# Optimization experiments

Hardware: AMD Instinct MI355X
Metric: run time of the kernel (lower is better)

Reference implementation:

```python
import jax, jax.numpy as jnp
import numpy as np


def _gcn_conv(x, W, b, src, dst, num_nodes):
    # PyG GCNConv: h = x @ W; symmetric normalization with self-loops; scatter-add; + bias
    h = x @ W
    deg = jax.ops.segment_sum(jnp.ones_like(dst, dtype=h.dtype), dst, num_segments=num_nodes)
    dinv = jnp.where(deg > 0, jax.lax.rsqrt(deg), 0.0)
    norm = dinv[src] * dinv[dst]                         # [E]
    msgs = h[src] * norm[:, None]                        # [E, H] gather + scale
    out = jax.ops.segment_sum(msgs, dst, num_segments=num_nodes)
    return out + b


def setup_inputs() -> dict:
    key = jax.random.key(0)
    ks = jax.random.split(key, 10)
    N, E = 500000, 1000000
    IN, H, SIG = 3, 64, 24
    x = jax.random.uniform(ks[0], (N, IN), dtype=jnp.float32)
    edge_index = jax.random.randint(ks[1], (2, E), 0, N, dtype=jnp.int64)
    batch = jnp.zeros((N,), dtype=jnp.int64)
    def glorot(k, shape):
        lim = np.sqrt(6.0 / (shape[0] + shape[1]))
        return jax.random.uniform(k, shape, dtype=jnp.float32, minval=-lim, maxval=lim)
    return {
        "x": x,
        "edge_index": edge_index,
        "batch": batch,
        "W1": glorot(ks[2], (IN, H)), "b1": jnp.zeros((H,), jnp.float32),
        "W2": glorot(ks[3], (H, H)),  "b2": jnp.zeros((H,), jnp.float32),
        "W3": glorot(ks[4], (H, H)),  "b3": jnp.zeros((H,), jnp.float32),
        "Wfc": glorot(ks[5], (H, SIG)), "bfc": jnp.zeros((SIG,), jnp.float32),
    }


def reference(x, edge_index, batch, W1, b1, W2, b2, W3, b3, Wfc, bfc):
    N = x.shape[0]
    NUM_GRAPHS = 1  # batch is all zeros (single graph)
    # add self-loops once (GCNConv adds them per layer; identical edge set each layer)
    loop = jnp.arange(N, dtype=edge_index.dtype)
    src = jnp.concatenate([edge_index[0], loop])
    dst = jnp.concatenate([edge_index[1], loop])

    h = jax.nn.relu(_gcn_conv(x, W1, b1, src, dst, N))
    h = jax.nn.relu(_gcn_conv(h, W2, b2, src, dst, N))
    h = jax.nn.relu(_gcn_conv(h, W3, b3, src, dst, N))

    # global mean pool per graph
    sums = jax.ops.segment_sum(h, batch, num_segments=NUM_GRAPHS)          # [G, H]
    counts = jax.ops.segment_sum(jnp.ones((N,), h.dtype), batch, num_segments=NUM_GRAPHS)
    sig = sums / jnp.maximum(counts, 1.0)[:, None]

    return jnp.tanh(sig @ Wfc + bfc)  # [G, 24]
```

## Files before the change

### kernel.cpp

```cpp
#include <hip/hip_runtime.h>
#include <hip/hip_bf16.h>
#include <hip/hip_fp16.h>


#define ALIGN256(x) (((x) + 255) & ~(size_t)255)
#define NBUCK_MAX 512

typedef _Float16 half8 __attribute__((ext_vector_type(8)));
typedef _Float16 half4 __attribute__((ext_vector_type(4)));
typedef float f32x4 __attribute__((ext_vector_type(4)));
typedef int i32x4 __attribute__((ext_vector_type(4)));

__device__ __forceinline__ void dec16(i32x4 r, half8& a, half8& b) {
    i32x4 u, v;
    u.x = (int)(((unsigned)r.x << 8) & 0xFF00FF00u);
    u.y = (int)(((unsigned)r.x)      & 0xFF00FF00u);
    u.z = (int)(((unsigned)r.y << 8) & 0xFF00FF00u);
    u.w = (int)(((unsigned)r.y)      & 0xFF00FF00u);
    v.x = (int)(((unsigned)r.z << 8) & 0xFF00FF00u);
    v.y = (int)(((unsigned)r.z)      & 0xFF00FF00u);
    v.z = (int)(((unsigned)r.w << 8) & 0xFF00FF00u);
    v.w = (int)(((unsigned)r.w)      & 0xFF00FF00u);
    a = *(half8*)&u; b = *(half8*)&v;
}

__device__ __forceinline__ unsigned char enc8(float x) {
    unsigned short hb = __half_as_ushort(__float2half(x));
    return (unsigned char)((hb + 0x80u) >> 8);
}

__global__ __launch_bounds__(256) void hist_kernel(const int* __restrict__ ei, int E, int CE, int SH,
                                                   int* __restrict__ cnt_mat,
                                                   float* __restrict__ pool,
                                                   unsigned char* __restrict__ h8a,
                                                   unsigned char* __restrict__ h8b, int N) {
    __shared__ int h[NBUCK_MAX];
    const int t = threadIdx.x, blk = blockIdx.x;
    if (blk == 0) {
        if (t < 64) pool[t] = 0.f;
        if (t < 16) {
            ((int*)(h8a + (size_t)N * 64))[t] = 0;
            ((int*)(h8b + (size_t)N * 64))[t] = 0;
        }
    }
    for (int i = t; i < NBUCK_MAX; i += 256) h[i] = 0;
    __syncthreads();
    const int e0 = blk * CE, e1 = min(E, e0 + CE);
    for (int e = e0 + t; e < e1; e += 256)
        atomicAdd(&h[ei[E + e] >> SH], 1);
    __syncthreads();
    for (int i = t; i < NBUCK_MAX; i += 256) cnt_mat[blk * NBUCK_MAX + i] = h[i];
}

__global__ __launch_bounds__(256) void scan_kernel(const int* __restrict__ cnt_mat,
                                                   int* __restrict__ base_mat,
                                                   int* __restrict__ startb, int nchunk, int NBK) {
    __shared__ int tots[NBUCK_MAX];
    const int t = threadIdx.x;
    for (int j = t; j < NBK; j += 256) {
        int run = 0;
        for (int b = 0; b < nchunk; ++b) {
            int v = cnt_mat[b * NBUCK_MAX + j];
            base_mat[b * NBUCK_MAX + j] = run;
            run += v;
        }
        tots[j] = run;
    }
    __syncthreads();
    if (t == 0) {
        int run = 0;
        for (int j = 0; j < NBK; ++j) { int v = tots[j]; startb[j] = run; run += v; }
        startb[NBK] = run;
    }
}

__global__ __launch_bounds__(256) void scatter_kernel(const int* __restrict__ ei, int E, int CE, int SH,
                                                      const int* __restrict__ base_mat,
                                                      const int* __restrict__ start,
                                                      unsigned* __restrict__ bkt) {
    __shared__ int sbuf[4096];
    __shared__ unsigned short sb[4096];
    __shared__ int lh[NBUCK_MAX];
    __shared__ int lbase[NBUCK_MAX];
    __shared__ int cur[NBUCK_MAX];
    __shared__ int ls[256];
    const int t = threadIdx.x, blk = blockIdx.x;
    for (int i = t; i < NBUCK_MAX; i += 256) { lh[i] = 0; cur[i] = 0; }
    __syncthreads();
    const int e0 = blk * CE, e1 = min(E, e0 + CE);
    for (int e = e0 + t; e < e1; e += 256)
        atomicAdd(&lh[ei[E + e] >> SH], 1);
    __syncthreads();
    int a0 = lh[2 * t], a1 = lh[2 * t + 1];
    ls[t] = a0 + a1;
    __syncthreads();
    if (t == 0) {
        int run = 0;
        for (int k = 0; k < 256; ++k) { int v = ls[k]; ls[k] = run; run += v; }
    }
    __syncthreads();
    lbase[2 * t]     = ls[t];
    lbase[2 * t + 1] = ls[t] + a0;
    __syncthreads();
    const unsigned lowm = (1u << SH) - 1u;
    for (int e = e0 + t; e < e1; e += 256) {
        int s = ei[e], d = ei[E + e];
        int b = d >> SH;
        int r = atomicAdd(&cur[b], 1);
        int slot = lbase[b] + r;
        sbuf[slot] = (int)((((unsigned)d & lowm) << 21) | (unsigned)s);
        sb[slot] = (unsigned short)b;
    }
    __syncthreads();
    const int n = e1 - e0;
    for (int i = t; i < n; i += 256) {
        int b = sb[i];
        int dest = start[b] + base_mat[blk * NBUCK_MAX + b] + (i - lbase[b]);
        bkt[dest] = (unsigned)sbuf[i];
    }
}

__global__ __launch_bounds__(256) void build_kernel(const unsigned* __restrict__ bkt,
                                                    const int* __restrict__ start,
                                                    int SH, int nrows, int N,
                                                    const float* __restrict__ x,
                                                    int* __restrict__ ell, int* __restrict__ sec,
                                                    half4* __restrict__ xs) {
    __shared__ __align__(16) int loc[2048][8];
    const int t = threadIdx.x, j = blockIdx.x;
    const int R = 1 << SH;
    int4 z = make_int4(0, 0, 0, 0);
    for (int i = t; i < R * 2; i += 256) ((int4*)loc)[i] = z;
    __syncthreads();
    const int s0 = start[j], s1 = start[j + 1];
    for (int e = s0 + t; e < s1; e += 256) {
        unsigned p = bkt[e];
        int dl = (int)(p >> 21);
        int src = (int)(p & 0x1FFFFFu);
        int k = atomicAdd(&loc[dl][0], 1);
        if (k < 7) loc[dl][1 + k] = src;
        else if (k < 15) {
            int grow = (j << SH) + dl;
            sec[(size_t)grow * 8 + (k - 7)] = src;
        }
    }
    __syncthreads();
    const int base = j << SH;
    for (int i = t; i < R; i += 256) {
        int grow = base + i;
        if (grow < nrows) {
            int4* dst = (int4*)(ell + (size_t)grow * 8);
            dst[0] = ((int4*)&loc[i][0])[0];
            dst[1] = ((int4*)&loc[i][0])[1];
            if (grow < N) {
                float d = rsqrtf((float)(loc[i][0] + 1));
                half4 v;
                v[0] = (_Float16)(d * x[(size_t)grow * 3 + 0]);
                v[1] = (_Float16)(d * x[(size_t)grow * 3 + 1]);
                v[2] = (_Float16)(d * x[(size_t)grow * 3 + 2]);
                v[3] = (_Float16)0.f;
                xs[grow] = v;
            } else if (grow == N) {
                *(int2*)&xs[N] = make_int2(0, 0);
            }
        }
    }
}

__global__ __launch_bounds__(256) void layer1_kernel(const half4* __restrict__ xs,
                                                     const int* __restrict__ ell,
                                                     const int* __restrict__ sec,
                                                     const float* __restrict__ W1, const float* __restrict__ b1,
                                                     unsigned char* __restrict__ hout, int N) {
    __shared__ float4 a1S[256];
    const int t = threadIdx.x;
    const int jg = blockIdx.x * 256 + t;
    const bool valid = (jg < N);
    const int jc = valid ? jg : N;

    half4 sv = xs[jc];
    float sx = (float)sv[0], sy = (float)sv[1], sz = (float)sv[2];
    const int* row = ell + (size_t)(valid ? jg : 0) * 8;
    int4 e0 = *(const int4*)row;
    int4 e1 = *(const int4*)(row + 4);
    int craw = valid ? e0.x : 0;
    int deg = min(craw, 15);
    int i0 = (deg > 0) ? e0.y : N;
    int i1 = (deg > 1) ? e0.z : N;
    int i2 = (deg > 2) ? e0.w : N;
    int i3 = (deg > 3) ? e1.x : N;
    int i4 = (deg > 4) ? e1.y : N;
    int i5 = (deg > 5) ? e1.z : N;
    int i6 = (deg > 6) ? e1.w : N;
    half4 q0 = xs[i0], q1 = xs[i1], q2 = xs[i2], q3 = xs[i3];
    half4 q4 = xs[i4], q5 = xs[i5], q6 = xs[i6];
    sx += (float)q0[0] + (float)q1[0] + (float)q2[0] + (float)q3[0]
        + (float)q4[0] + (float)q5[0] + (float)q6[0];
    sy += (float)q0[1] + (float)q1[1] + (float)q2[1] + (float)q3[1]
        + (float)q4[1] + (float)q5[1] + (float)q6[1];
    sz += (float)q0[2] + (float)q1[2] + (float)q2[2] + (float)q3[2]
        + (float)q4[2] + (float)q5[2] + (float)q6[2];
    if (deg > 7) {
        const int* srow = sec + (size_t)jg * 8;
        for (int i = 7; i < deg; ++i) {
            half4 qq = xs[srow[i - 7]];
            sx += (float)qq[0]; sy += (float)qq[1]; sz += (float)qq[2];
        }
    }
    float dj = valid ? rsqrtf((float)(craw + 1)) : 0.f;
    a1S[t] = make_float4(dj * sx, dj * sy, dj * sz, dj);
    __syncthreads();

    const int l = t & 63, w = t >> 6;
    const float w0 = W1[l], w1 = W1[64 + l], w2 = W1[128 + l], bl = b1[l];
    const int base = blockIdx.x * 256 + w * 64;
    #pragma unroll 4
    for (int n = 0; n < 64; ++n) {
        int j2 = base + n;
        if (j2 >= N) break;
        float4 a = a1S[w * 64 + n];
        float v = fmaf(a.x, w0, fmaf(a.y, w1, fmaf(a.z, w2, bl)));
        hout[(size_t)j2 * 64 + l] = enc8(a.w * fmaxf(v, 0.f));
    }
}

template <int POOL>
__global__ __launch_bounds__(256) void layer_kernel(const unsigned char* __restrict__ hin,
                                                    const int* __restrict__ ell,
                                                    const int* __restrict__ sec,
                                                    const float* __restrict__ W, const float* __restrict__ bias,
                                                    unsigned char* __restrict__ hout, float* __restrict__ pool, int N) {
    const int t = threadIdx.x;
    const int l = t & 63;
    const int w = t >> 6;
    const int l15 = l & 15, q = l >> 4;
    const int m = l >> 2, qq = l & 3;
    const int cbase = l & ~3;

    __shared__ float red[256];
    __shared__ __align__(16) _Float16 wlds[8 * 64 * 8];
    __shared__ __align__(16) int tbuf[4][16 * 36];

    for (int c = t; c < 512; c += 256) {
        int f = c >> 6, ln = c & 63;
        int ct = f >> 1, kt = f & 1;
        int q2 = ln >> 4, m2 = ln & 15;
        half8 b;
        #pragma unroll
        for (int j = 0; j < 8; ++j) {
            int g = 4 * q2 + (j >> 1);
            int ii = g & 7, blk = g >> 3;
            int feat = 16 * blk + 4 * (ii >> 1) + (ii & 1) + 2 * (j & 1);
            b[j] = (_Float16)W[(kt * 32 + feat) * 64 + ct * 16 + m2];
        }
        *(half8*)&wlds[(size_t)c * 8] = b;
    }
    float bb[4];
    #pragma unroll
    for (int ct = 0; ct < 4; ++ct) bb[ct] = bias[ct * 16 + l15];
    __syncthreads();

    const char* hb = (const char*)hin;
    const int vlo = qq * 16;
    float ps0 = 0.f, ps1 = 0.f, ps2 = 0.f, ps3 = 0.f;

    const int ngroups = (N + 15) >> 4;
    const int gstride = gridDim.x * 4;
    for (int g = blockIdx.x * 4 + w; g < ngroups; g += gstride) {
        const int j0 = g << 4;
        const int jm = j0 + m;
        const bool validm = (jm < N);
        const int jsm = validm ? jm : N;

        i32x4 iv = *(const i32x4*)(ell + (size_t)jsm * 8 + (qq & 1) * 4);

        int cnt = __shfl(iv.x, cbase, 64);
        int s1  = __shfl(iv.y, cbase, 64);
        int s2  = __shfl(iv.z, cbase, 64);
        int s3  = __shfl(iv.w, cbase, 64);
        int s4  = __shfl(iv.x, cbase + 1, 64);
        int s5  = __shfl(iv.y, cbase + 1, 64);
        int s6  = __shfl(iv.z, cbase + 1, 64);
        int s7  = __shfl(iv.w, cbase + 1, 64);

        int craw = validm ? cnt : 0;
        int degc = min(craw, 15);
        float djv = rsqrtf((float)(craw + 1));

        int dmax = degc;
        dmax = max(dmax, __shfl_xor(dmax, 4, 64));
        dmax = max(dmax, __shfl_xor(dmax, 8, 64));
        dmax = max(dmax, __shfl_xor(dmax, 16, 64));
        dmax = max(dmax, __shfl_xor(dmax, 32, 64));

        s1 = (degc > 0) ? s1 : N;
        s2 = (degc > 1) ? s2 : N;
        s3 = (degc > 2) ? s3 : N;
        s4 = (degc > 3) ? s4 : N;
        s5 = (degc > 4) ? s5 : N;
        s6 = (degc > 5) ? s6 : N;
        s7 = (degc > 6) ? s7 : N;

        i32x4 rS = *(const i32x4*)(hb + ((size_t)jsm << 6) + vlo);
        i32x4 r1 = *(const i32x4*)(hb + ((size_t)(unsigned)s1 << 6) + vlo);
        i32x4 r2 = *(const i32x4*)(hb + ((size_t)(unsigned)s2 << 6) + vlo);
        i32x4 r3 = *(const i32x4*)(hb + ((size_t)(unsigned)s3 << 6) + vlo);
        i32x4 r4 = *(const i32x4*)(hb + ((size_t)(unsigned)s4 << 6) + vlo);
        const bool big = (dmax > 4);
        i32x4 r5, r6, r7;
        if (big) {
            r5 = *(const i32x4*)(hb + ((size_t)(unsigned)s5 << 6) + vlo);
            r6 = *(const i32x4*)(hb + ((size_t)(unsigned)s6 << 6) + vlo);
            r7 = *(const i32x4*)(hb + ((size_t)(unsigned)s7 << 6) + vlo);
        }

        half8 aA, aB, tA, tB;
        dec16(rS, aA, aB);
        dec16(r1, tA, tB); aA += tA; aB += tB;
        dec16(r2, tA, tB); aA += tA; aB += tB;
        dec16(r3, tA, tB); aA += tA; aB += tB;
        dec16(r4, tA, tB); aA += tA; aB += tB;
        if (big) {
            dec16(r5, tA, tB); aA += tA; aB += tB;
            dec16(r6, tA, tB); aA += tA; aB += tB;
            dec16(r7, tA, tB); aA += tA; aB += tB;
        }
        if (dmax > 7) {
            const int* srow = sec + (size_t)jsm * 8;
            #pragma unroll
            for (int ww = 8; ww < 16; ++ww) {
                int sr = (degc > ww - 1) ? srow[ww - 8] : N;
                i32x4 rt = *(const i32x4*)(hb + ((size_t)(unsigned)sr << 6) + vlo);
                dec16(rt, tA, tB); aA += tA; aB += tB;
            }
        }

        *(i32x4*)&tbuf[w][m * 36 + qq * 8]     = *(i32x4*)&aA;
        *(i32x4*)&tbuf[w][m * 36 + qq * 8 + 4] = *(i32x4*)&aB;
        half8 af0 = *(half8*)&tbuf[w][l15 * 36 + 4 * q];
        half8 af1 = *(half8*)&tbuf[w][l15 * 36 + 16 + 4 * q];

        const half8* wl = (const half8*)wlds;
        f32x4 c0 = {0.f, 0.f, 0.f, 0.f}, c1 = c0, c2 = c0, c3 = c0;
        c0 = __builtin_amdgcn_mfma_f32_16x16x32_f16(af0, wl[      l], c0, 0, 0, 0);
        c1 = __builtin_amdgcn_mfma_f32_16x16x32_f16(af0, wl[128 + l], c1, 0, 0, 0);
        c2 = __builtin_amdgcn_mfma_f32_16x16x32_f16(af0, wl[256 + l], c2, 0, 0, 0);
        c3 = __builtin_amdgcn_mfma_f32_16x16x32_f16(af0, wl[384 + l], c3, 0, 0, 0);
        c0 = __builtin_amdgcn_mfma_f32_16x16x32_f16(af1, wl[ 64 + l], c0, 0, 0, 0);
        c1 = __builtin_amdgcn_mfma_f32_16x16x32_f16(af1, wl[192 + l], c1, 0, 0, 0);
        c2 = __builtin_amdgcn_mfma_f32_16x16x32_f16(af1, wl[320 + l], c2, 0, 0, 0);
        c3 = __builtin_amdgcn_mfma_f32_16x16x32_f16(af1, wl[448 + l], c3, 0, 0, 0);

        if (POOL) {
            #pragma unroll
            for (int r = 0; r < 4; ++r) {
                int row = q * 4 + r;
                int gj = j0 + row;
                float djr = __shfl(djv, row << 2, 64);
                if (gj < N) {
                    ps0 += fmaxf(djr * c0[r] + bb[0], 0.f);
                    ps1 += fmaxf(djr * c1[r] + bb[1], 0.f);
                    ps2 += fmaxf(djr * c2[r] + bb[2], 0.f);
                    ps3 += fmaxf(djr * c3[r] + bb[3], 0.f);
                }
            }
        } else {
            #pragma unroll
            for (int r = 0; r < 4; ++r) {
                int row = q * 4 + r;
                int gj = j0 + row;
                float djr = __shfl(djv, row << 2, 64);
                if (gj < N) {
                    unsigned char* hp = hout + (size_t)gj * 64 + l15;
                    hp[0]  = enc8(djr * fmaxf(djr * c0[r] + bb[0], 0.f));
                    hp[16] = enc8(djr * fmaxf(djr * c1[r] + bb[1], 0.f));
                    hp[32] = enc8(djr * fmaxf(djr * c2[r] + bb[2], 0.f));
                    hp[48] = enc8(djr * fmaxf(djr * c3[r] + bb[3], 0.f));
                }
            }
        }
    }

    if (POOL) {
        ps0 += __shfl_xor(ps0, 16, 64); ps0 += __shfl_xor(ps0, 32, 64);
        ps1 += __shfl_xor(ps1, 16, 64); ps1 += __shfl_xor(ps1, 32, 64);
        ps2 += __shfl_xor(ps2, 16, 64); ps2 += __shfl_xor(ps2, 32, 64);
        ps3 += __shfl_xor(ps3, 16, 64); ps3 += __shfl_xor(ps3, 32, 64);
        if (q == 0) {
            red[w * 64 + l15]      = ps0;
            red[w * 64 + 16 + l15] = ps1;
            red[w * 64 + 32 + l15] = ps2;
            red[w * 64 + 48 + l15] = ps3;
        }
        __syncthreads();
        if (t < 64) {
            float s = red[t] + red[64 + t] + red[128 + t] + red[192 + t];
            atomicAdd(&pool[t], s);
        }
    }
}

__global__ __launch_bounds__(64) void final_kernel(const float* __restrict__ pool, const float* __restrict__ Wfc,
                                                   const float* __restrict__ bfc, float* __restrict__ out, int N) {
    int t = threadIdx.x;
    if (t < 24) {
        float inv = 1.0f / (float)N;
        float s = bfc[t];
        for (int c = 0; c < 64; ++c) s += pool[c] * inv * Wfc[c * 24 + t];
        out[t] = tanhf(s);
    }
}

extern "C" void kernel_launch(void* const* d_in, const int* in_sizes, int n_in,
                              void* d_out, int out_size, void* d_ws, size_t ws_size,
                              hipStream_t stream) {
    const float* x   = (const float*)d_in[0];
    const int*   ei  = (const int*)d_in[1];
    const float* W1  = (const float*)d_in[3];
    const float* b1  = (const float*)d_in[4];
    const float* W2  = (const float*)d_in[5];
    const float* b2  = (const float*)d_in[6];
    const float* W3  = (const float*)d_in[7];
    const float* b3  = (const float*)d_in[8];
    const float* Wfc = (const float*)d_in[9];
    const float* bfc = (const float*)d_in[10];
    float* out = (float*)d_out;

    const int N = in_sizes[2];
    const int E = in_sizes[1] / 2;

    size_t off = 0;
    auto take = [&](size_t bytes) -> char* {
        char* p = (char*)d_ws + off;
        off = ALIGN256(off + bytes);
        return p;
    };
    const int nrows = N + 16;
    int SH = 11;
    while ((((nrows - 1) >> SH) + 1) > NBUCK_MAX) ++SH;
    const int NBK = ((nrows - 1) >> SH) + 1;
    const int NCHUNK = (E + 4095) / 4096;
    const int CE = (E + NCHUNK - 1) / NCHUNK;

    int*           ell     = (int*)     take((size_t)nrows * 8 * 4);
    int*           sec     = (int*)     take((size_t)nrows * 8 * 4);
    unsigned*      bkt     = (unsigned*)take((size_t)E * 4);
    int*           cnt_mat = (int*)     take((size_t)NBUCK_MAX * NBUCK_MAX * 4);
    int*           base_mat= (int*)     take((size_t)NBUCK_MAX * NBUCK_MAX * 4);
    int*           startb  = (int*)     take((NBUCK_MAX + 1) * 4);
    float*         pool    = (float*)   take(64 * 4);
    half4*         xs      = (half4*)   take(((size_t)N + 1) * 8);
    unsigned char* h8a     = (unsigned char*)take((size_t)(N + 1) * 64);
    unsigned char* h8b     = (unsigned char*)take((size_t)(N + 1) * 64);
    (void)ws_size; (void)n_in; (void)out_size;

    hist_kernel<<<NCHUNK, 256, 0, stream>>>(ei, E, CE, SH, cnt_mat, pool, h8a, h8b, N);
    scan_kernel<<<1, 256, 0, stream>>>(cnt_mat, base_mat, startb, NCHUNK, NBK);
    scatter_kernel<<<NCHUNK, 256, 0, stream>>>(ei, E, CE, SH, base_mat, startb, bkt);
    build_kernel<<<NBK, 256, 0, stream>>>(bkt, startb, SH, nrows, N, x, ell, sec, xs);

    layer1_kernel<<<(N + 255) / 256, 256, 0, stream>>>(xs, ell, sec, W1, b1, h8a, N);

    int LB = 1024;
    const int ngroups = (N + 15) >> 4;
    const int maxb = (ngroups + 3) / 4;
    if (LB > maxb) LB = maxb;

    layer_kernel<0><<<LB, 256, 0, stream>>>(h8a, ell, sec, W2, b2, h8b, nullptr, N);

    layer_kernel<1><<<LB, 256, 0, stream>>>(h8b, ell, sec, W3, b3, nullptr, pool, N);

    final_kernel<<<1, 64, 0, stream>>>(pool, Wfc, bfc, out, N);
}
```

Before: 282.4 us.

## Parallelize bucket-offset scan across blocks with two-level column scan

```diff
diff --git a/kernel.cpp b/kernel.cpp
--- a/kernel.cpp
+++ b/kernel.cpp
@@ -52,26 +52,50 @@
     for (int i = t; i < NBUCK_MAX; i += 256) cnt_mat[blk * NBUCK_MAX + i] = h[i];
 }
 
-__global__ __launch_bounds__(256) void scan_kernel(const int* __restrict__ cnt_mat,
-                                                   int* __restrict__ base_mat,
-                                                   int* __restrict__ startb, int nchunk, int NBK) {
-    __shared__ int tots[NBUCK_MAX];
+__global__ __launch_bounds__(64) void colscan_kernel(const int* __restrict__ cnt_mat,
+                                                     int* __restrict__ base_mat,
+                                                     int* __restrict__ tot, int nblk) {
+    __shared__ int ls[64];
+    const int j = blockIdx.x;
     const int t = threadIdx.x;
-    for (int j = t; j < NBK; j += 256) {
-        int run = 0;
-        for (int b = 0; b < nchunk; ++b) {
-            int v = cnt_mat[b * NBUCK_MAX + j];
-            base_mat[b * NBUCK_MAX + j] = run;
-            run += v;
-        }
-        tots[j] = run;
-    }
+    const int PER = (nblk + 63) >> 6;
+    const int b0 = t * PER, b1 = min(nblk, b0 + PER);
+    int s = 0;
+    for (int b = b0; b < b1; ++b) s += cnt_mat[b * NBUCK_MAX + j];
+    ls[t] = s;
     __syncthreads();
     if (t == 0) {
         int run = 0;
-        for (int j = 0; j < NBK; ++j) { int v = tots[j]; startb[j] = run; run += v; }
-        startb[NBK] = run;
-    }
+        for (int k = 0; k < 64; ++k) { int v = ls[k]; ls[k] = run; run += v; }
+        tot[j] = run;
+    }
+    __syncthreads();
+    int run = ls[t];
+    for (int b = b0; b < b1; ++b) {
+        int v = cnt_mat[b * NBUCK_MAX + j];
+        base_mat[b * NBUCK_MAX + j] = run;
+        run += v;
+    }
+}
+
+__global__ __launch_bounds__(256) void totscan_kernel(const int* __restrict__ tot,
+                                                      int* __restrict__ startb, int NBK, int E) {
+    __shared__ int ls[256];
+    const int t = threadIdx.x;
+    const int PER = (NBK + 255) >> 8;
+    const int j0 = t * PER, j1 = min(NBK, j0 + PER);
+    int s = 0;
+    for (int j = j0; j < j1; ++j) s += tot[j];
+    ls[t] = s;
+    __syncthreads();
+    if (t == 0) {
+        int run = 0;
+        for (int k = 0; k < 256; ++k) { int v = ls[k]; ls[k] = run; run += v; }
+        startb[NBK] = E;
+    }
+    __syncthreads();
+    int run = ls[t];
+    for (int j = j0; j < j1; ++j) { startb[j] = run; run += tot[j]; }
 }
 
 __global__ __launch_bounds__(256) void scatter_kernel(const int* __restrict__ ei, int E, int CE, int SH,
@@ -447,6 +471,7 @@
     unsigned*      bkt     = (unsigned*)take((size_t)E * 4);
     int*           cnt_mat = (int*)     take((size_t)NBUCK_MAX * NBUCK_MAX * 4);
     int*           base_mat= (int*)     take((size_t)NBUCK_MAX * NBUCK_MAX * 4);
+    int*           tot     = (int*)     take(NBUCK_MAX * 4);
     int*           startb  = (int*)     take((NBUCK_MAX + 1) * 4);
     float*         pool    = (float*)   take(64 * 4);
     half4*         xs      = (half4*)   take(((size_t)N + 1) * 8);
@@ -455,7 +480,8 @@
     (void)ws_size; (void)n_in; (void)out_size;
 
     hist_kernel<<<NCHUNK, 256, 0, stream>>>(ei, E, CE, SH, cnt_mat, pool, h8a, h8b, N);
-    scan_kernel<<<1, 256, 0, stream>>>(cnt_mat, base_mat, startb, NCHUNK, NBK);
+    colscan_kernel<<<NBK, 64, 0, stream>>>(cnt_mat, base_mat, tot, NCHUNK);
+    totscan_kernel<<<1, 256, 0, stream>>>(tot, startb, NBK, E);
     scatter_kernel<<<NCHUNK, 256, 0, stream>>>(ei, E, CE, SH, base_mat, startb, bkt);
     build_kernel<<<NBK, 256, 0, stream>>>(bkt, startb, SH, nrows, N, x, ell, sec, xs);
 
```

Result: faster. 228.9 us, median of 2 (-18.9%).
